# Kernel tuning notes

Measured on AMD Instinct MI355X. Metric: run time of the kernel, lower is better.

Reference implementation:

```python
import jax, jax.numpy as jnp
import numpy as np
from jax.scipy.special import erfc

# Constants baked into PmeModule.__init__ (NNPOps PME)
GRID = (14, 15, 16)          # reciprocal mesh
ORDER = 5                    # B-spline order
ALPHA = 4.985823141035867    # Ewald splitting parameter (1/nm)
COULOMB = 138.935            # ONE_4PI_EPS0, kJ/mol*nm/e^2
CUTOFF = 0.5                 # direct-space cutoff (forward arg in source)
N_ATOMS = 4096


def _M(k, x):
    """Cardinal B-spline M_k evaluated elementwise (Essmann et al. 1995)."""
    if k == 1:
        return jnp.where((x >= 0.0) & (x < 1.0), 1.0, 0.0)
    return (x * _M(k - 1, x) + (k - x) * _M(k - 1, x - 1.0)) / (k - 1)


def _bspline_moduli(K):
    """|b(m)|^2 per axis; zero out ill-defined modes (odd order, m=K/2)."""
    m = jnp.arange(K)
    kk = jnp.arange(ORDER - 1, dtype=jnp.float32)
    Mv = _M(ORDER, kk + 1.0)                                   # M_n(1..n-1)
    ph = jnp.exp(2j * jnp.pi * m[:, None] * kk[None, :] / K)
    denom = (Mv[None, :] * ph).sum(-1)
    d2 = jnp.abs(denom) ** 2
    return jnp.where(d2 < 1e-7, 0.0, 1.0 / d2)


def _direct(positions, charges, box):
    # All-pairs minimum-image (triclinic-reduced) erfc/r sum within cutoff.
    delta = positions[:, None, :] - positions[None, :, :]      # [N,N,3]
    for a in (2, 1, 0):
        delta = delta - box[a] * jnp.round(delta[..., a:a + 1] / box[a, a])
    r2 = (delta ** 2).sum(-1)                                  # [N,N]
    n = positions.shape[0]
    mask = (r2 < CUTOFF ** 2) & ~jnp.eye(n, dtype=bool)
    r = jnp.sqrt(jnp.where(mask, r2, 1.0))
    qq = charges[:, None] * charges[None, :]
    e = jnp.where(mask, qq * erfc(ALPHA * r) / r, 0.0)
    return 0.5 * COULOMB * e.sum()                             # each pair once


def _spread(positions, charges, box):
    """Spread charges onto the mesh with order-5 B-splines (periodic)."""
    frac = positions @ jnp.linalg.inv(box)                     # fractional coords
    frac = frac - jnp.floor(frac)                              # wrap to [0,1)
    u = frac * jnp.array(GRID, jnp.float32)                    # [N,3]
    base = jnp.floor(u)
    w = u - base
    offs = jnp.arange(ORDER, dtype=jnp.float32)
    wts = _M(ORDER, w[:, :, None] + offs[None, None, :])       # [N,3,ORDER]
    idx = (base.astype(jnp.int32)[:, :, None]
           - jnp.arange(ORDER, dtype=jnp.int32)[None, None, :]) \
          % jnp.array(GRID, jnp.int32)[None, :, None]          # [N,3,ORDER]
    wq = (charges[:, None, None, None] * wts[:, 0, :, None, None]
          * wts[:, 1, None, :, None] * wts[:, 2, None, None, :])  # [N,5,5,5]
    fi = (idx[:, 0, :, None, None] * (GRID[1] * GRID[2])
          + idx[:, 1, None, :, None] * GRID[2]
          + idx[:, 2, None, None, :])                          # flat indices
    g = jnp.zeros(GRID[0] * GRID[1] * GRID[2], positions.dtype)
    return g.at[fi.reshape(-1)].add(wq.reshape(-1)).reshape(GRID)


def _reciprocal(positions, charges, box):
    Q = _spread(positions, charges, box)
    F = jnp.fft.fftn(Q)
    recip = jnp.linalg.inv(box)                                # recip vecs = columns
    mx = jnp.fft.fftfreq(GRID[0]) * GRID[0]
    my = jnp.fft.fftfreq(GRID[1]) * GRID[1]
    mz = jnp.fft.fftfreq(GRID[2]) * GRID[2]
    mv = (mx[:, None, None, None] * recip.T[0]
          + my[None, :, None, None] * recip.T[1]
          + mz[None, None, :, None] * recip.T[2])              # [Kx,Ky,Kz,3]
    m2 = (mv ** 2).sum(-1)
    B = (_bspline_moduli(GRID[0])[:, None, None]
         * _bspline_moduli(GRID[1])[None, :, None]
         * _bspline_moduli(GRID[2])[None, None, :])
    nz = m2 > 0.0
    m2s = jnp.where(nz, m2, 1.0)
    green = jnp.where(nz, jnp.exp(-(jnp.pi ** 2) * m2s / ALPHA ** 2) / m2s, 0.0)
    V = jnp.abs(jnp.linalg.det(box))
    erec = COULOMB / (2.0 * jnp.pi * V) * (green * B * jnp.abs(F) ** 2).sum()
    eself = -COULOMB * ALPHA / jnp.sqrt(jnp.pi) * (charges ** 2).sum()
    return erec + eself


def setup_inputs() -> dict:
    key = jax.random.key(0)
    k1, k2 = jax.random.split(key)
    box = jnp.diag(jnp.array([3.0, 3.1, 3.2], jnp.float32))    # nm, diagonal box
    positions = jax.random.uniform(k1, (N_ATOMS, 3), jnp.float32) * jnp.diag(box)
    charges = 0.5 * jax.random.normal(k2, (N_ATOMS,), jnp.float32)
    return {"positions": positions, "charges": charges, "box_vectors": box}


def reference(positions, charges, box_vectors):
    edir = _direct(positions, charges, box_vectors)
    erecip = _reciprocal(positions, charges, box_vectors)
    return edir - erecip
```

## Files before the change

kernel.cpp:

```cpp
#include <hip/hip_runtime.h>
#include <math.h>

#define NATOM 4096
#define KX 14
#define KY 15
#define KZ 16
#define SLAB (KY*KZ)
#define NGRID (KX*SLAB)
#define NB 128
#define APB (NATOM/NB)
#define NTRI 544

static constexpr float ALPHA_F   = 4.985823141035867f;
static constexpr float COULOMB_F = 138.935f;
static constexpr float CUT2_F    = 0.25f;
static constexpr float TWOPI_F   = 6.283185307179586f;
static constexpr float PI_F      = 3.14159265358979f;

#define POIS32 0xAAAAAAAAu
#define CTR_LAST (POIS32 + 15u)

__device__ __forceinline__ float M1f(float x){ return (x >= 0.f && x < 1.f) ? 1.f : 0.f; }
__device__ __forceinline__ float M2f(float x){ return x*M1f(x) + (2.f-x)*M1f(x-1.f); }
__device__ __forceinline__ float M3f(float x){ return (x*M2f(x) + (3.f-x)*M2f(x-1.f)) * 0.5f; }
__device__ __forceinline__ float M4f(float x){ return (x*M3f(x) + (4.f-x)*M3f(x-1.f)) * (1.f/3.f); }
__device__ __forceinline__ float M5f(float x){ return (x*M4f(x) + (5.f-x)*M4f(x-1.f)) * 0.25f; }

__device__ __forceinline__ void inv3x3(const float* b, float* inv){
  float det = b[0]*(b[4]*b[8]-b[5]*b[7]) - b[1]*(b[3]*b[8]-b[5]*b[6]) + b[2]*(b[3]*b[7]-b[4]*b[6]);
  float id = 1.f/det;
  inv[0] = (b[4]*b[8]-b[5]*b[7])*id;
  inv[1] = (b[2]*b[7]-b[1]*b[8])*id;
  inv[2] = (b[1]*b[5]-b[2]*b[4])*id;
  inv[3] = (b[5]*b[6]-b[3]*b[8])*id;
  inv[4] = (b[0]*b[8]-b[2]*b[6])*id;
  inv[5] = (b[2]*b[3]-b[0]*b[5])*id;
  inv[6] = (b[3]*b[7]-b[4]*b[6])*id;
  inv[7] = (b[1]*b[6]-b[0]*b[7])*id;
  inv[8] = (b[0]*b[4]-b[1]*b[3])*id;
}

__device__ __forceinline__ float bmod(int m, int K){
  float base = TWOPI_F * (float)m / (float)K;
  float s, c;
  float dr = 1.f/24.f, di = 0.f;
  __sincosf(base,      &s, &c); dr += (11.f/24.f)*c; di += (11.f/24.f)*s;
  __sincosf(base*2.f,  &s, &c); dr += (11.f/24.f)*c; di += (11.f/24.f)*s;
  __sincosf(base*3.f,  &s, &c); dr += (1.f/24.f)*c;  di += (1.f/24.f)*s;
  float d2 = dr*dr + di*di;
  return (d2 < 1e-7f) ? 0.f : 1.f/d2;
}

__device__ __forceinline__ float erfc_poly(float x){
  float tt = __builtin_amdgcn_rcpf(1.f + 0.3275911f*x);
  return ((((1.061405429f*tt - 1.453152027f)*tt + 1.421413741f)*tt
          - 0.284496736f)*tt + 0.254829592f)*tt;
}

__global__ __launch_bounds__(256) void fat_kernel(const float* __restrict__ pos,
    const float* __restrict__ chg, const float* __restrict__ box,
    float* __restrict__ grid, double* __restrict__ dpart)
{
  __shared__ float sg[NGRID];
  __shared__ float sx[64], sy[64], sz[64], sw[64];
  __shared__ double red4[4];
  int t = threadIdx.x;
  int b = blockIdx.x;

  if (b < NB){
    int sb = b;
    for (int i = t; i < NGRID; i += 256) sg[i] = 0.f;
    __syncthreads();

    if (t < APB*5){
      int a   = t / 5;
      int jxi = t - 5*a;
      int atom = sb*APB + a;
      float bx[9], inv[9];
      #pragma unroll
      for (int i = 0; i < 9; ++i) bx[i] = box[i];
      inv3x3(bx, inv);

      float px = pos[atom*3+0], py = pos[atom*3+1], pz = pos[atom*3+2];
      float qi = chg[atom];
      float fr[3];
      fr[0] = px*inv[0] + py*inv[3] + pz*inv[6];
      fr[1] = px*inv[1] + py*inv[4] + pz*inv[7];
      fr[2] = px*inv[2] + py*inv[5] + pz*inv[8];

      const int Ks[3] = {KX, KY, KZ};
      float w[3][5]; int id[3][5];
      #pragma unroll
      for (int ax = 0; ax < 3; ++ax) {
        float f = fr[ax] - floorf(fr[ax]);
        float u = f * (float)Ks[ax];
        float bse = floorf(u);
        float x = u - bse;
        int bi = (int)bse;
        #pragma unroll
        for (int j = 0; j < 5; ++j) {
          w[ax][j] = M5f(x + (float)j);
          int ii = bi - j; if (ii < 0) ii += Ks[ax];
          id[ax][j] = ii;
        }
      }
      float qx = qi * w[0][jxi];
      int ox = id[0][jxi]*SLAB;
      #pragma unroll
      for (int jy = 0; jy < 5; ++jy) {
        float qxy = qx * w[1][jy];
        int oxy = ox + id[1][jy]*KZ;
        #pragma unroll
        for (int jz = 0; jz < 5; ++jz)
          atomicAdd(&sg[oxy + id[2][jz]], qxy * w[2][jz]);
      }
    }
    __syncthreads();
    int base = (sb * 1051) % NGRID;
    for (int i0 = t; i0 < NGRID; i0 += 256){
      int i = i0 + base; if (i >= NGRID) i -= NGRID;
      float v = sg[i];
      if (v != 0.f) atomicAdd(&grid[i], v);
    }

  } else {
    int rem = b - NB, ci = 0;
    while (true){ int cnt = 64 - 4*ci; if (rem < cnt) break; rem -= cnt; ++ci; }
    int cj = 4*ci + rem;
    bool offdiag = (rem >= 4);
    int i  = ci*256 + t;
    int j0 = cj*64;
    if (t < 64){
      int j = j0 + t;
      sx[t] = pos[j*3+0]; sy[t] = pos[j*3+1]; sz[t] = pos[j*3+2]; sw[t] = chg[j];
    }
    __syncthreads();

    float b00=box[0],b01=box[1],b02=box[2],
          b10=box[3],b11=box[4],b12=box[5],
          b20=box[6],b21=box[7],b22=box[8];
    bool diag = (b01==0.f && b02==0.f && b10==0.f && b12==0.f && b20==0.f && b21==0.f);
    float i00 = 1.f/b00, i11 = 1.f/b11, i22 = 1.f/b22;

    float xi = pos[i*3+0], yi = pos[i*3+1], zi = pos[i*3+2], qi = chg[i];
    const float A2 = ALPHA_F*ALPHA_F;
    float e = 0.f;

    if (diag){
      #pragma unroll 4
      for (int jj = 0; jj < 64; ++jj){
        float dx = xi - sx[jj], dy = yi - sy[jj], dz = zi - sz[jj];
        dz -= b22*rintf(dz*i22);
        dy -= b11*rintf(dy*i11);
        dx -= b00*rintf(dx*i00);
        float r2 = dx*dx + dy*dy + dz*dz;
        if (r2 < CUT2_F && (j0 + jj) != i){
          float rinv = __builtin_amdgcn_rsqf(r2);
          float x = ALPHA_F * (r2 * rinv);
          e += qi * sw[jj] * erfc_poly(x) * __expf(-A2*r2) * rinv;
        }
      }
    } else {
      for (int jj = 0; jj < 64; ++jj){
        float dx = xi - sx[jj], dy = yi - sy[jj], dz = zi - sz[jj];
        float t2 = rintf(dz * i22); dx -= b20*t2; dy -= b21*t2; dz -= b22*t2;
        float t1 = rintf(dy * i11); dx -= b10*t1; dy -= b11*t1; dz -= b12*t1;
        float t0 = rintf(dx * i00); dx -= b00*t0; dy -= b01*t0; dz -= b02*t0;
        float r2 = dx*dx + dy*dy + dz*dz;
        if (r2 < CUT2_F && (j0 + jj) != i){
          float rinv = __builtin_amdgcn_rsqf(r2);
          float x = ALPHA_F * (r2 * rinv);
          e += qi * sw[jj] * erfc_poly(x) * __expf(-A2*r2) * rinv;
        }
      }
    }

    double de = (double)e;
    #pragma unroll
    for (int off = 32; off > 0; off >>= 1) de += __shfl_down(de, off);
    if ((t & 63) == 0) red4[t >> 6] = de;
    __syncthreads();
    if (t == 0){
      double s = red4[0]+red4[1]+red4[2]+red4[3];
      dpart[b - NB] = offdiag ? 2.0*s : s;
    }
  }
}

__global__ __launch_bounds__(256) void recip_kernel(const float* __restrict__ grid,
    const float* __restrict__ chg, const float* __restrict__ box,
    const double* __restrict__ dpart, double* __restrict__ acc_rec,
    unsigned* __restrict__ ctr, float* __restrict__ out)
{
  __shared__ float2 Ty[KY*KY];
  __shared__ float2 Tx[KX*KX];
  __shared__ float2 Cz[KX*KY];
  __shared__ float2 Cyv[KX*KY];
  __shared__ double red[12];
  __shared__ int lastflag;
  int t  = threadIdx.x;
  int mz = blockIdx.x;
  const float P = __uint_as_float(POIS32);

  if (t < KY*KY){
    int my = t / KY, gy = t % KY;
    float s, c; __sincosf(-TWOPI_F*(float)((my*gy)%KY)/(float)KY, &s, &c);
    Ty[t] = make_float2(c, s);
  }
  if (t < KX*KX){
    int mx = t / KX, gx = t % KX;
    float s, c; __sincosf(-TWOPI_F*(float)((mx*gx)%KX)/(float)KX, &s, &c);
    Tx[t] = make_float2(c, s);
  }

  int u = t;
  if (u < KX*KY){
    const float4* g4 = (const float4*)grid;
    float q[16];
    #pragma unroll
    for (int k = 0; k < 4; ++k){
      float4 v = g4[u*4 + k];
      q[4*k+0] = v.x - P; q[4*k+1] = v.y - P; q[4*k+2] = v.z - P; q[4*k+3] = v.w - P;
    }
    float br = 0.f, bi = 0.f;
    #pragma unroll
    for (int gz = 0; gz < KZ; ++gz){
      float s, c; __sincosf(-TWOPI_F*(float)((mz*gz)%KZ)/(float)KZ, &s, &c);
      br += q[gz]*c; bi += q[gz]*s;
    }
    Cz[u] = make_float2(br, bi);
  }
  __syncthreads();

  if (u < KX*KY){
    int gx = u / KY, my = u % KY;
    float ar = 0.f, ai = 0.f;
    #pragma unroll
    for (int gy = 0; gy < KY; ++gy){
      float2 v = Cz[gx*KY + gy];
      float2 w = Ty[my*KY + gy];
      ar += v.x*w.x - v.y*w.y;
      ai += v.x*w.y + v.y*w.x;
    }
    Cyv[u] = make_float2(ar, ai);
  }
  __syncthreads();

  double s_rec = 0.0;
  if (u < KX*KY){
    int mx = u / KY, my = u % KY;
    float Fr = 0.f, Fi = 0.f;
    #pragma unroll
    for (int gx = 0; gx < KX; ++gx){
      float2 v = Cyv[gx*KY + my];
      float2 w = Tx[mx*KX + gx];
      Fr += v.x*w.x - v.y*w.y;
      Fi += v.x*w.y + v.y*w.x;
    }
    float bx[9], inv[9];
    #pragma unroll
    for (int k = 0; k < 9; ++k) bx[k] = box[k];
    inv3x3(bx, inv);
    float fx = (mx <= (KX-1)/2) ? (float)mx : (float)(mx - KX);
    float fy = (my <= (KY-1)/2) ? (float)my : (float)(my - KY);
    float fz = (mz <= (KZ-1)/2) ? (float)mz : (float)(mz - KZ);
    float mv0 = fx*inv[0] + fy*inv[1] + fz*inv[2];
    float mv1 = fx*inv[3] + fy*inv[4] + fz*inv[5];
    float mv2 = fx*inv[6] + fy*inv[7] + fz*inv[8];
    float m2 = mv0*mv0 + mv1*mv1 + mv2*mv2;
    float B  = bmod(mx,KX)*bmod(my,KY)*bmod(mz,KZ);
    if (m2 > 0.f && B > 0.f){
      float green = __expf(-(PI_F*PI_F)*m2/(ALPHA_F*ALPHA_F)) / m2;
      s_rec = (double)(green*B) * ((double)Fr*(double)Fr + (double)Fi*(double)Fi);
    }
  }

  #pragma unroll
  for (int off = 32; off > 0; off >>= 1) s_rec += __shfl_down(s_rec, off);
  int lane = t & 63, wid = t >> 6;
  if (lane == 0) red[wid] = s_rec;
  __syncthreads();
  if (t == 0){
    atomicAdd(acc_rec, red[0]+red[1]+red[2]+red[3]);
    asm volatile("s_waitcnt vmcnt(0)" ::: "memory");
    unsigned old = __hip_atomic_fetch_add(ctr, 1u, __ATOMIC_RELAXED, __HIP_MEMORY_SCOPE_AGENT);
    lastflag = (old == CTR_LAST) ? 1 : 0;
  }
  __syncthreads();

  if (lastflag){
    double s_dir = dpart[t] + dpart[t+256] + ((t < NTRI-512) ? dpart[t+512] : 0.0);
    double s_q2 = 0.0;
    #pragma unroll
    for (int i = t; i < NATOM; i += 256){ double q = (double)chg[i]; s_q2 += q*q; }
    #pragma unroll
    for (int off = 32; off > 0; off >>= 1){
      s_dir += __shfl_down(s_dir, off);
      s_q2  += __shfl_down(s_q2,  off);
    }
    if (lane == 0){ red[4+wid] = s_dir; red[8+wid] = s_q2; }
    __syncthreads();
    if (t == 0){
      double D = red[4]+red[5]+red[6]+red[7];
      double Q = red[8]+red[9]+red[10]+red[11];
      double R = __hip_atomic_load(acc_rec, __ATOMIC_ACQUIRE, __HIP_MEMORY_SCOPE_AGENT);
      double b00=box[0],b01=box[1],b02=box[2],
             b10=box[3],b11=box[4],b12=box[5],
             b20=box[6],b21=box[7],b22=box[8];
      double det = b00*(b11*b22 - b12*b21) - b01*(b10*b22 - b12*b20) + b02*(b10*b21 - b11*b20);
      double V = fabs(det);
      const double PI_D = 3.141592653589793238462643;
      double edir  = 0.5 * (double)COULOMB_F * D;
      double erec  = (double)COULOMB_F / (2.0*PI_D*V) * R;
      double eself = -(double)COULOMB_F * 4.985823141035867 / sqrt(PI_D) * Q;
      out[0] = (float)(edir - erec - eself);
    }
  }
}

extern "C" void kernel_launch(void* const* d_in, const int* in_sizes, int n_in,
                              void* d_out, int out_size, void* d_ws, size_t ws_size,
                              hipStream_t stream) {
  const float* pos = (const float*)d_in[0];
  const float* chg = (const float*)d_in[1];
  const float* box = (const float*)d_in[2];
  float* out = (float*)d_out;

  char* w = (char*)d_ws;
  float*    grid    = (float*)w;
  double*   dpart   = (double*)(w + 16384);
  double*   acc_rec = (double*)(w + 24576);
  unsigned* ctr     = (unsigned*)(w + 24584);

  fat_kernel<<<NB + NTRI, 256, 0, stream>>>(pos, chg, box, grid, dpart);
  recip_kernel<<<KZ, 256, 0, stream>>>(grid, chg, box, dpart, acc_rec, ctr, out);
}
```

Baseline: 79.26 us.

## Move direct-space pair work into the reciprocal kernel's launch

Splits the old fused kernel so charge spreading runs alone, and moves the direct-space pair blocks into the second launch alongside the 16 reciprocal blocks. Direct sums are now accumulated with a double atomic, and the last-block counter covers all blocks. The intent is to shorten the critical path: the short spread kernel finishes first, then the 16-block FFT stage overlaps with the heavy direct-space work instead of running serially after it. The cost is contention on a single double atomic and a counter that 560 blocks must hit.

```diff
diff --git a/kernel.cpp b/kernel.cpp
--- a/kernel.cpp
+++ b/kernel.cpp
@@ -10,6 +10,7 @@
 #define NB 128
 #define APB (NATOM/NB)
 #define NTRI 544
+#define NMIX (16 + NTRI)
 
 static constexpr float ALPHA_F   = 4.985823141035867f;
 static constexpr float COULOMB_F = 138.935f;
@@ -18,7 +19,7 @@
 static constexpr float PI_F      = 3.14159265358979f;
 
 #define POIS32 0xAAAAAAAAu
-#define CTR_LAST (POIS32 + 15u)
+#define CTR_LAST (POIS32 + (unsigned)(NMIX - 1))
 
 __device__ __forceinline__ float M1f(float x){ return (x >= 0.f && x < 1.f) ? 1.f : 0.f; }
 __device__ __forceinline__ float M2f(float x){ return x*M1f(x) + (2.f-x)*M1f(x-1.f); }
@@ -57,74 +58,176 @@
           - 0.284496736f)*tt + 0.254829592f)*tt;
 }
 
-__global__ __launch_bounds__(256) void fat_kernel(const float* __restrict__ pos,
+__global__ __launch_bounds__(256) void spread_kernel(const float* __restrict__ pos,
     const float* __restrict__ chg, const float* __restrict__ box,
-    float* __restrict__ grid, double* __restrict__ dpart)
+    float* __restrict__ grid)
 {
   __shared__ float sg[NGRID];
+  int t = threadIdx.x;
+  int sb = blockIdx.x;
+
+  for (int i = t; i < NGRID; i += 256) sg[i] = 0.f;
+  __syncthreads();
+
+  if (t < APB*5){
+    int a   = t / 5;
+    int jxi = t - 5*a;
+    int atom = sb*APB + a;
+    float bx[9], inv[9];
+    #pragma unroll
+    for (int i = 0; i < 9; ++i) bx[i] = box[i];
+    inv3x3(bx, inv);
+
+    float px = pos[atom*3+0], py = pos[atom*3+1], pz = pos[atom*3+2];
+    float qi = chg[atom];
+    float fr[3];
+    fr[0] = px*inv[0] + py*inv[3] + pz*inv[6];
+    fr[1] = px*inv[1] + py*inv[4] + pz*inv[7];
+    fr[2] = px*inv[2] + py*inv[5] + pz*inv[8];
+
+    const int Ks[3] = {KX, KY, KZ};
+    float w[3][5]; int id[3][5];
+    #pragma unroll
+    for (int ax = 0; ax < 3; ++ax) {
+      float f = fr[ax] - floorf(fr[ax]);
+      float u = f * (float)Ks[ax];
+      float bse = floorf(u);
+      float x = u - bse;
+      int bi = (int)bse;
+      #pragma unroll
+      for (int j = 0; j < 5; ++j) {
+        w[ax][j] = M5f(x + (float)j);
+        int ii = bi - j; if (ii < 0) ii += Ks[ax];
+        id[ax][j] = ii;
+      }
+    }
+    float qx = qi * w[0][jxi];
+    int ox = id[0][jxi]*SLAB;
+    #pragma unroll
+    for (int jy = 0; jy < 5; ++jy) {
+      float qxy = qx * w[1][jy];
+      int oxy = ox + id[1][jy]*KZ;
+      #pragma unroll
+      for (int jz = 0; jz < 5; ++jz)
+        atomicAdd(&sg[oxy + id[2][jz]], qxy * w[2][jz]);
+    }
+  }
+  __syncthreads();
+  int base = (sb * 1051) % NGRID;
+  for (int i0 = t; i0 < NGRID; i0 += 256){
+    int i = i0 + base; if (i >= NGRID) i -= NGRID;
+    float v = sg[i];
+    if (v != 0.f) atomicAdd(&grid[i], v);
+  }
+}
+
+__global__ __launch_bounds__(256) void mix_kernel(const float* __restrict__ pos,
+    const float* __restrict__ chg, const float* __restrict__ box,
+    const float* __restrict__ grid, double* __restrict__ acc_rec,
+    double* __restrict__ acc_dir, unsigned* __restrict__ ctr,
+    float* __restrict__ out)
+{
+  __shared__ float2 Ty[KY*KY];
+  __shared__ float2 Tx[KX*KX];
+  __shared__ float2 Cz[KX*KY];
+  __shared__ float2 Cyv[KX*KY];
   __shared__ float sx[64], sy[64], sz[64], sw[64];
-  __shared__ double red4[4];
+  __shared__ double red[12];
+  __shared__ int lastflag;
   int t = threadIdx.x;
   int b = blockIdx.x;
-
-  if (b < NB){
-    int sb = b;
-    for (int i = t; i < NGRID; i += 256) sg[i] = 0.f;
-    __syncthreads();
-
-    if (t < APB*5){
-      int a   = t / 5;
-      int jxi = t - 5*a;
-      int atom = sb*APB + a;
+  int lane = t & 63, wid = t >> 6;
+  const float P = __uint_as_float(POIS32);
+
+  if (b < 16){
+    int mz = b;
+    if (t < KY*KY){
+      int my = t / KY, gy = t % KY;
+      float s, c; __sincosf(-TWOPI_F*(float)((my*gy)%KY)/(float)KY, &s, &c);
+      Ty[t] = make_float2(c, s);
+    }
+    if (t < KX*KX){
+      int mx = t / KX, gx = t % KX;
+      float s, c; __sincosf(-TWOPI_F*(float)((mx*gx)%KX)/(float)KX, &s, &c);
+      Tx[t] = make_float2(c, s);
+    }
+
+    int u = t;
+    if (u < KX*KY){
+      const float4* g4 = (const float4*)grid;
+      float q[16];
+      #pragma unroll
+      for (int k = 0; k < 4; ++k){
+        float4 v = g4[u*4 + k];
+        q[4*k+0] = v.x - P; q[4*k+1] = v.y - P; q[4*k+2] = v.z - P; q[4*k+3] = v.w - P;
+      }
+      float br = 0.f, bi = 0.f;
+      #pragma unroll
+      for (int gz = 0; gz < KZ; ++gz){
+        float s, c; __sincosf(-TWOPI_F*(float)((mz*gz)%KZ)/(float)KZ, &s, &c);
+        br += q[gz]*c; bi += q[gz]*s;
+      }
+      Cz[u] = make_float2(br, bi);
+    }
+    __syncthreads();
+
+    if (u < KX*KY){
+      int gx = u / KY, my = u % KY;
+      float ar = 0.f, ai = 0.f;
+      #pragma unroll
+      for (int gy = 0; gy < KY; ++gy){
+        float2 v = Cz[gx*KY + gy];
+        float2 w = Ty[my*KY + gy];
+        ar += v.x*w.x - v.y*w.y;
+        ai += v.x*w.y + v.y*w.x;
+      }
+      Cyv[u] = make_float2(ar, ai);
+    }
+    __syncthreads();
+
+    double s_rec = 0.0;
+    if (u < KX*KY){
+      int mx = u / KY, my = u % KY;
+      float Fr = 0.f, Fi = 0.f;
+      #pragma unroll
+      for (int gx = 0; gx < KX; ++gx){
+        float2 v = Cyv[gx*KY + my];
+        float2 w = Tx[mx*KX + gx];
+        Fr += v.x*w.x - v.y*w.y;
+        Fi += v.x*w.y + v.y*w.x;
+      }
       float bx[9], inv[9];
       #pragma unroll
-      for (int i = 0; i < 9; ++i) bx[i] = box[i];
+      for (int k = 0; k < 9; ++k) bx[k] = box[k];
       inv3x3(bx, inv);
-
-      float px = pos[atom*3+0], py = pos[atom*3+1], pz = pos[atom*3+2];
-      float qi = chg[atom];
-      float fr[3];
-      fr[0] = px*inv[0] + py*inv[3] + pz*inv[6];
-      fr[1] = px*inv[1] + py*inv[4] + pz*inv[7];
-      fr[2] = px*inv[2] + py*inv[5] + pz*inv[8];
-
-      const int Ks[3] = {KX, KY, KZ};
-      float w[3][5]; int id[3][5];
-      #pragma unroll
-      for (int ax = 0; ax < 3; ++ax) {
-        float f = fr[ax] - floorf(fr[ax]);
-        float u = f * (float)Ks[ax];
-        float bse = floorf(u);
-        float x = u - bse;
-        int bi = (int)bse;
-        #pragma unroll
-        for (int j = 0; j < 5; ++j) {
-          w[ax][j] = M5f(x + (float)j);
-          int ii = bi - j; if (ii < 0) ii += Ks[ax];
-          id[ax][j] = ii;
-        }
-      }
-      float qx = qi * w[0][jxi];
-      int ox = id[0][jxi]*SLAB;
-      #pragma unroll
-      for (int jy = 0; jy < 5; ++jy) {
-        float qxy = qx * w[1][jy];
-        int oxy = ox + id[1][jy]*KZ;
-        #pragma unroll
-        for (int jz = 0; jz < 5; ++jz)
-          atomicAdd(&sg[oxy + id[2][jz]], qxy * w[2][jz]);
-      }
-    }
-    __syncthreads();
-    int base = (sb * 1051) % NGRID;
-    for (int i0 = t; i0 < NGRID; i0 += 256){
-      int i = i0 + base; if (i >= NGRID) i -= NGRID;
-      float v = sg[i];
-      if (v != 0.f) atomicAdd(&grid[i], v);
-    }
+      float fx = (mx <= (KX-1)/2) ? (float)mx : (float)(mx - KX);
+      float fy = (my <= (KY-1)/2) ? (float)my : (float)(my - KY);
+      float fz = (mz <= (KZ-1)/2) ? (float)mz : (float)(mz - KZ);
+      float mv0 = fx*inv[0] + fy*inv[1] + fz*inv[2];
+      float mv1 = fx*inv[3] + fy*inv[4] + fz*inv[5];
+      float mv2 = fx*inv[6] + fy*inv[7] + fz*inv[8];
+      float m2 = mv0*mv0 + mv1*mv1 + mv2*mv2;
+      float B  = bmod(mx,KX)*bmod(my,KY)*bmod(mz,KZ);
+      if (m2 > 0.f && B > 0.f){
+        float green = __expf(-(PI_F*PI_F)*m2/(ALPHA_F*ALPHA_F)) / m2;
+        s_rec = (double)(green*B) * ((double)Fr*(double)Fr + (double)Fi*(double)Fi);
+      }
+    }
+
+    #pragma unroll
+    for (int off = 32; off > 0; off >>= 1) s_rec += __shfl_down(s_rec, off);
+    if (lane == 0) red[wid] = s_rec;
+    __syncthreads();
+    if (t == 0){
+      atomicAdd(acc_rec, red[0]+red[1]+red[2]+red[3]);
+      asm volatile("s_waitcnt vmcnt(0)" ::: "memory");
+      unsigned old = __hip_atomic_fetch_add(ctr, 1u, __ATOMIC_RELAXED, __HIP_MEMORY_SCOPE_AGENT);
+      lastflag = (old == CTR_LAST) ? 1 : 0;
+    }
+    __syncthreads();
 
   } else {
-    int rem = b - NB, ci = 0;
+    int rem = b - 16, ci = 0;
     while (true){ int cnt = 64 - 4*ci; if (rem < cnt) break; rem -= cnt; ++ci; }
     int cj = 4*ci + rem;
     bool offdiag = (rem >= 4);
@@ -178,132 +281,31 @@
     double de = (double)e;
     #pragma unroll
     for (int off = 32; off > 0; off >>= 1) de += __shfl_down(de, off);
-    if ((t & 63) == 0) red4[t >> 6] = de;
+    if (lane == 0) red[wid] = de;
     __syncthreads();
     if (t == 0){
-      double s = red4[0]+red4[1]+red4[2]+red4[3];
-      dpart[b - NB] = offdiag ? 2.0*s : s;
-    }
+      double s = red[0]+red[1]+red[2]+red[3];
+      atomicAdd(acc_dir, offdiag ? 2.0*s : s);
+      asm volatile("s_waitcnt vmcnt(0)" ::: "memory");
+      unsigned old = __hip_atomic_fetch_add(ctr, 1u, __ATOMIC_RELAXED, __HIP_MEMORY_SCOPE_AGENT);
+      lastflag = (old == CTR_LAST) ? 1 : 0;
+    }
+    __syncthreads();
   }
-}
-
-__global__ __launch_bounds__(256) void recip_kernel(const float* __restrict__ grid,
-    const float* __restrict__ chg, const float* __restrict__ box,
-    const double* __restrict__ dpart, double* __restrict__ acc_rec,
-    unsigned* __restrict__ ctr, float* __restrict__ out)
-{
-  __shared__ float2 Ty[KY*KY];
-  __shared__ float2 Tx[KX*KX];
-  __shared__ float2 Cz[KX*KY];
-  __shared__ float2 Cyv[KX*KY];
-  __shared__ double red[12];
-  __shared__ int lastflag;
-  int t  = threadIdx.x;
-  int mz = blockIdx.x;
-  const float P = __uint_as_float(POIS32);
-
-  if (t < KY*KY){
-    int my = t / KY, gy = t % KY;
-    float s, c; __sincosf(-TWOPI_F*(float)((my*gy)%KY)/(float)KY, &s, &c);
-    Ty[t] = make_float2(c, s);
-  }
-  if (t < KX*KX){
-    int mx = t / KX, gx = t % KX;
-    float s, c; __sincosf(-TWOPI_F*(float)((mx*gx)%KX)/(float)KX, &s, &c);
-    Tx[t] = make_float2(c, s);
-  }
-
-  int u = t;
-  if (u < KX*KY){
-    const float4* g4 = (const float4*)grid;
-    float q[16];
-    #pragma unroll
-    for (int k = 0; k < 4; ++k){
-      float4 v = g4[u*4 + k];
-      q[4*k+0] = v.x - P; q[4*k+1] = v.y - P; q[4*k+2] = v.z - P; q[4*k+3] = v.w - P;
-    }
-    float br = 0.f, bi = 0.f;
-    #pragma unroll
-    for (int gz = 0; gz < KZ; ++gz){
-      float s, c; __sincosf(-TWOPI_F*(float)((mz*gz)%KZ)/(float)KZ, &s, &c);
-      br += q[gz]*c; bi += q[gz]*s;
-    }
-    Cz[u] = make_float2(br, bi);
-  }
-  __syncthreads();
-
-  if (u < KX*KY){
-    int gx = u / KY, my = u % KY;
-    float ar = 0.f, ai = 0.f;
-    #pragma unroll
-    for (int gy = 0; gy < KY; ++gy){
-      float2 v = Cz[gx*KY + gy];
-      float2 w = Ty[my*KY + gy];
-      ar += v.x*w.x - v.y*w.y;
-      ai += v.x*w.y + v.y*w.x;
-    }
-    Cyv[u] = make_float2(ar, ai);
-  }
-  __syncthreads();
-
-  double s_rec = 0.0;
-  if (u < KX*KY){
-    int mx = u / KY, my = u % KY;
-    float Fr = 0.f, Fi = 0.f;
-    #pragma unroll
-    for (int gx = 0; gx < KX; ++gx){
-      float2 v = Cyv[gx*KY + my];
-      float2 w = Tx[mx*KX + gx];
-      Fr += v.x*w.x - v.y*w.y;
-      Fi += v.x*w.y + v.y*w.x;
-    }
-    float bx[9], inv[9];
-    #pragma unroll
-    for (int k = 0; k < 9; ++k) bx[k] = box[k];
-    inv3x3(bx, inv);
-    float fx = (mx <= (KX-1)/2) ? (float)mx : (float)(mx - KX);
-    float fy = (my <= (KY-1)/2) ? (float)my : (float)(my - KY);
-    float fz = (mz <= (KZ-1)/2) ? (float)mz : (float)(mz - KZ);
-    float mv0 = fx*inv[0] + fy*inv[1] + fz*inv[2];
-    float mv1 = fx*inv[3] + fy*inv[4] + fz*inv[5];
-    float mv2 = fx*inv[6] + fy*inv[7] + fz*inv[8];
-    float m2 = mv0*mv0 + mv1*mv1 + mv2*mv2;
-    float B  = bmod(mx,KX)*bmod(my,KY)*bmod(mz,KZ);
-    if (m2 > 0.f && B > 0.f){
-      float green = __expf(-(PI_F*PI_F)*m2/(ALPHA_F*ALPHA_F)) / m2;
-      s_rec = (double)(green*B) * ((double)Fr*(double)Fr + (double)Fi*(double)Fi);
-    }
-  }
-
-  #pragma unroll
-  for (int off = 32; off > 0; off >>= 1) s_rec += __shfl_down(s_rec, off);
-  int lane = t & 63, wid = t >> 6;
-  if (lane == 0) red[wid] = s_rec;
-  __syncthreads();
-  if (t == 0){
-    atomicAdd(acc_rec, red[0]+red[1]+red[2]+red[3]);
-    asm volatile("s_waitcnt vmcnt(0)" ::: "memory");
-    unsigned old = __hip_atomic_fetch_add(ctr, 1u, __ATOMIC_RELAXED, __HIP_MEMORY_SCOPE_AGENT);
-    lastflag = (old == CTR_LAST) ? 1 : 0;
-  }
-  __syncthreads();
 
   if (lastflag){
-    double s_dir = dpart[t] + dpart[t+256] + ((t < NTRI-512) ? dpart[t+512] : 0.0);
+    __threadfence();
     double s_q2 = 0.0;
     #pragma unroll
     for (int i = t; i < NATOM; i += 256){ double q = (double)chg[i]; s_q2 += q*q; }
     #pragma unroll
-    for (int off = 32; off > 0; off >>= 1){
-      s_dir += __shfl_down(s_dir, off);
-      s_q2  += __shfl_down(s_q2,  off);
-    }
-    if (lane == 0){ red[4+wid] = s_dir; red[8+wid] = s_q2; }
+    for (int off = 32; off > 0; off >>= 1) s_q2 += __shfl_down(s_q2, off);
+    if (lane == 0) red[4+wid] = s_q2;
     __syncthreads();
     if (t == 0){
-      double D = red[4]+red[5]+red[6]+red[7];
-      double Q = red[8]+red[9]+red[10]+red[11];
+      double Q = red[4]+red[5]+red[6]+red[7];
       double R = __hip_atomic_load(acc_rec, __ATOMIC_ACQUIRE, __HIP_MEMORY_SCOPE_AGENT);
+      double D = __hip_atomic_load(acc_dir, __ATOMIC_ACQUIRE, __HIP_MEMORY_SCOPE_AGENT);
       double b00=box[0],b01=box[1],b02=box[2],
              b10=box[3],b11=box[4],b12=box[5],
              b20=box[6],b21=box[7],b22=box[8];
@@ -328,10 +330,10 @@
 
   char* w = (char*)d_ws;
   float*    grid    = (float*)w;
-  double*   dpart   = (double*)(w + 16384);
-  double*   acc_rec = (double*)(w + 24576);
-  unsigned* ctr     = (unsigned*)(w + 24584);
-
-  fat_kernel<<<NB + NTRI, 256, 0, stream>>>(pos, chg, box, grid, dpart);
-  recip_kernel<<<KZ, 256, 0, stream>>>(grid, chg, box, dpart, acc_rec, ctr, out);
-}
+  double*   acc_rec = (double*)(w + 16384);
+  double*   acc_dir = (double*)(w + 16392);
+  unsigned* ctr     = (unsigned*)(w + 16400);
+
+  spread_kernel<<<NB, 256, 0, stream>>>(pos, chg, box, grid);
+  mix_kernel<<<NMIX, 256, 0, stream>>>(pos, chg, box, grid, acc_rec, acc_dir, ctr, out);
+}
```

After: 94.65 us. 1.19x slower.
